# Performance work log

Measured on AMD Instinct MI355X. Metric: run time of the kernel, lower is better.

Reference implementation:

```python
import jax, jax.numpy as jnp
import numpy as np

B, C_IN, H, W = 32, 12, 495, 436
C_HID = 16


def setup_inputs() -> dict:
    key = jax.random.key(0)
    k_x, k1, k2, k3, kb1, kb2, kb3 = jax.random.split(key, 7)
    x = jax.random.uniform(k_x, (B, C_IN, H, W), dtype=jnp.float32) * 255.0
    # Kaiming-uniform-ish init; exact distribution irrelevant for a correctness baseline.
    def u(k, shape, fan_in):
        bound = 1.0 / np.sqrt(fan_in)
        return jax.random.uniform(k, shape, dtype=jnp.float32, minval=-bound, maxval=bound)
    w1 = u(k1, (C_HID, C_IN), C_IN)   # conv1 1x1 kernel [out, in]
    b1 = u(kb1, (C_HID,), C_IN)
    w2 = u(k2, (C_HID, C_HID), C_HID)
    b2 = u(kb2, (C_HID,), C_HID)
    w3 = u(k3, (1, C_HID), C_HID)
    b3 = u(kb3, (1,), C_HID)
    return {"x": x, "w1": w1, "b1": b1, "w2": w2, "b2": b2, "w3": w3, "b3": b3}


def _conv1x1(x, w, b):
    # x: [B, Cin, H, W], w: [Cout, Cin], b: [Cout]
    return jnp.einsum("bchw,oc->bohw", x, w) + b[None, :, None, None]


def reference(x, w1, b1, w2, b2, w3, b3):
    h = x / 255.0 - 0.5
    h = jax.nn.relu(_conv1x1(h, w1, b1))
    h = jax.nn.relu(_conv1x1(h, w2, b2))
    h = jax.nn.sigmoid(_conv1x1(h, w3, b3))
    return 255.0 * h
```

## Files before the change

### kernel.cpp

```cpp
#include <hip/hip_runtime.h>
#include <math.h>

#define B_    32
#define C_IN  12
#define C_HID 16
#define H_    495
#define W_    436
#define HW    (H_ * W_)
#define NPIX  (B_ * HW)
#define NG    (NPIX / 4)

__global__ __launch_bounds__(256) void temporal_mlp_kernel(
    const float* __restrict__ x,
    const float* __restrict__ w1, const float* __restrict__ b1,
    const float* __restrict__ w2, const float* __restrict__ b2,
    const float* __restrict__ w3, const float* __restrict__ b3,
    float* __restrict__ out)
{
    __shared__ __align__(16) float sW1[16][12];
    __shared__ __align__(16) float sB1[16];
    __shared__ __align__(16) float sW2[16][16];
    __shared__ __align__(16) float sB2[16];
    __shared__ __align__(16) float sW3[16];
    __shared__ float sB3;

    const int tid = threadIdx.x;
    if (tid < 192) sW1[tid / 12][tid % 12] = w1[tid] * (1.0f / 255.0f);
    sW2[tid / 16][tid % 16] = w2[tid];
    if (tid < 16) {
        float s = 0.0f;
        #pragma unroll
        for (int c = 0; c < 12; ++c) s += w1[tid * 12 + c];
        sB1[tid] = b1[tid] - 0.5f * s;
        sB2[tid] = b2[tid];
        sW3[tid] = w3[tid];
    }
    if (tid == 0) sB3 = b3[0];
    __syncthreads();

    const int g = blockIdx.x * 256 + tid;
    if (g >= NG) return;

    const int base = g * 4;
    const int b    = base / HW;
    const int p    = base - b * HW;
    const float* xb = x + (size_t)b * (C_IN * HW) + p;

    float xin0[12], xin1[12], xin2[12], xin3[12];
    #pragma unroll
    for (int c = 0; c < 12; ++c) {
        float4 t = *(const float4*)(xb + (size_t)c * HW);
        xin0[c] = t.x; xin1[c] = t.y; xin2[c] = t.z; xin3[c] = t.w;
    }

    float h10[16], h11[16], h12[16], h13[16];
    #pragma unroll
    for (int o = 0; o < 16; ++o) {
        float wr[12];
        ((float4*)wr)[0] = ((const float4*)(&sW1[o][0]))[0];
        ((float4*)wr)[1] = ((const float4*)(&sW1[o][0]))[1];
        ((float4*)wr)[2] = ((const float4*)(&sW1[o][0]))[2];
        const float bb = sB1[o];
        float a0 = bb, a1 = bb, a2 = bb, a3 = bb;
        #pragma unroll
        for (int c = 0; c < 12; ++c) {
            a0 = fmaf(xin0[c], wr[c], a0);
            a1 = fmaf(xin1[c], wr[c], a1);
            a2 = fmaf(xin2[c], wr[c], a2);
            a3 = fmaf(xin3[c], wr[c], a3);
        }
        h10[o] = fmaxf(a0, 0.0f); h11[o] = fmaxf(a1, 0.0f);
        h12[o] = fmaxf(a2, 0.0f); h13[o] = fmaxf(a3, 0.0f);
    }

    float h20[16], h21[16], h22[16], h23[16];
    #pragma unroll
    for (int o = 0; o < 16; ++o) {
        float wr[16];
        ((float4*)wr)[0] = ((const float4*)(&sW2[o][0]))[0];
        ((float4*)wr)[1] = ((const float4*)(&sW2[o][0]))[1];
        ((float4*)wr)[2] = ((const float4*)(&sW2[o][0]))[2];
        ((float4*)wr)[3] = ((const float4*)(&sW2[o][0]))[3];
        const float bb = sB2[o];
        float a0 = bb, a1 = bb, a2 = bb, a3 = bb;
        #pragma unroll
        for (int c = 0; c < 16; ++c) {
            a0 = fmaf(h10[c], wr[c], a0);
            a1 = fmaf(h11[c], wr[c], a1);
            a2 = fmaf(h12[c], wr[c], a2);
            a3 = fmaf(h13[c], wr[c], a3);
        }
        h20[o] = fmaxf(a0, 0.0f); h21[o] = fmaxf(a1, 0.0f);
        h22[o] = fmaxf(a2, 0.0f); h23[o] = fmaxf(a3, 0.0f);
    }

    float wr[16];
    ((float4*)wr)[0] = ((const float4*)(&sW3[0]))[0];
    ((float4*)wr)[1] = ((const float4*)(&sW3[0]))[1];
    ((float4*)wr)[2] = ((const float4*)(&sW3[0]))[2];
    ((float4*)wr)[3] = ((const float4*)(&sW3[0]))[3];
    const float b3v = sB3;
    float t0 = b3v, t1 = b3v, t2 = b3v, t3 = b3v;
    #pragma unroll
    for (int c = 0; c < 16; ++c) {
        t0 = fmaf(h20[c], wr[c], t0);
        t1 = fmaf(h21[c], wr[c], t1);
        t2 = fmaf(h22[c], wr[c], t2);
        t3 = fmaf(h23[c], wr[c], t3);
    }
    float4 r;
    r.x = 255.0f / (1.0f + __expf(-t0));
    r.y = 255.0f / (1.0f + __expf(-t1));
    r.z = 255.0f / (1.0f + __expf(-t2));
    r.w = 255.0f / (1.0f + __expf(-t3));
    *(float4*)(out + base) = r;
}

extern "C" void kernel_launch(void* const* d_in, const int* in_sizes, int n_in,
                              void* d_out, int out_size, void* d_ws, size_t ws_size,
                              hipStream_t stream) {
    const float* x  = (const float*)d_in[0];
    const float* w1 = (const float*)d_in[1];
    const float* b1 = (const float*)d_in[2];
    const float* w2 = (const float*)d_in[3];
    const float* b2 = (const float*)d_in[4];
    const float* w3 = (const float*)d_in[5];
    const float* b3 = (const float*)d_in[6];
    float* out = (float*)d_out;

    const int grid = (NG + 255) / 256;
    temporal_mlp_kernel<<<grid, 256, 0, stream>>>(x, w1, b1, w2, b2, w3, b3, out);
}
```

Measured before the change: 451.9 us.

## Process two pixels per thread and read weights directly from global memory

```diff
diff --git a/kernel.cpp b/kernel.cpp
--- a/kernel.cpp
+++ b/kernel.cpp
@@ -8,7 +8,7 @@
 #define W_    436
 #define HW    (H_ * W_)
 #define NPIX  (B_ * HW)
-#define NG    (NPIX / 4)
+#define NG2   (NPIX / 2)
 
 __global__ __launch_bounds__(256) void temporal_mlp_kernel(
     const float* __restrict__ x,
@@ -17,103 +17,64 @@
     const float* __restrict__ w3, const float* __restrict__ b3,
     float* __restrict__ out)
 {
-    __shared__ __align__(16) float sW1[16][12];
-    __shared__ __align__(16) float sB1[16];
-    __shared__ __align__(16) float sW2[16][16];
-    __shared__ __align__(16) float sB2[16];
-    __shared__ __align__(16) float sW3[16];
-    __shared__ float sB3;
+    const int g = blockIdx.x * 256 + threadIdx.x;
+    if (g >= NG2) return;
 
-    const int tid = threadIdx.x;
-    if (tid < 192) sW1[tid / 12][tid % 12] = w1[tid] * (1.0f / 255.0f);
-    sW2[tid / 16][tid % 16] = w2[tid];
-    if (tid < 16) {
-        float s = 0.0f;
-        #pragma unroll
-        for (int c = 0; c < 12; ++c) s += w1[tid * 12 + c];
-        sB1[tid] = b1[tid] - 0.5f * s;
-        sB2[tid] = b2[tid];
-        sW3[tid] = w3[tid];
-    }
-    if (tid == 0) sB3 = b3[0];
-    __syncthreads();
-
-    const int g = blockIdx.x * 256 + tid;
-    if (g >= NG) return;
-
-    const int base = g * 4;
+    const int base = g * 2;
     const int b    = base / HW;
     const int p    = base - b * HW;
     const float* xb = x + (size_t)b * (C_IN * HW) + p;
 
-    float xin0[12], xin1[12], xin2[12], xin3[12];
+    float xn0[12], xn1[12];
     #pragma unroll
     for (int c = 0; c < 12; ++c) {
-        float4 t = *(const float4*)(xb + (size_t)c * HW);
-        xin0[c] = t.x; xin1[c] = t.y; xin2[c] = t.z; xin3[c] = t.w;
+        float2 t = *(const float2*)(xb + (size_t)c * HW);
+        xn0[c] = fmaf(t.x, 1.0f / 255.0f, -0.5f);
+        xn1[c] = fmaf(t.y, 1.0f / 255.0f, -0.5f);
     }
 
-    float h10[16], h11[16], h12[16], h13[16];
+    float h10[16], h11[16];
     #pragma unroll
     for (int o = 0; o < 16; ++o) {
-        float wr[12];
-        ((float4*)wr)[0] = ((const float4*)(&sW1[o][0]))[0];
-        ((float4*)wr)[1] = ((const float4*)(&sW1[o][0]))[1];
-        ((float4*)wr)[2] = ((const float4*)(&sW1[o][0]))[2];
-        const float bb = sB1[o];
-        float a0 = bb, a1 = bb, a2 = bb, a3 = bb;
+        const float bb = b1[o];
+        float a0 = bb, a1 = bb;
         #pragma unroll
         for (int c = 0; c < 12; ++c) {
-            a0 = fmaf(xin0[c], wr[c], a0);
-            a1 = fmaf(xin1[c], wr[c], a1);
-            a2 = fmaf(xin2[c], wr[c], a2);
-            a3 = fmaf(xin3[c], wr[c], a3);
+            const float w = w1[o * 12 + c];
+            a0 = fmaf(xn0[c], w, a0);
+            a1 = fmaf(xn1[c], w, a1);
         }
-        h10[o] = fmaxf(a0, 0.0f); h11[o] = fmaxf(a1, 0.0f);
-        h12[o] = fmaxf(a2, 0.0f); h13[o] = fmaxf(a3, 0.0f);
+        h10[o] = fmaxf(a0, 0.0f);
+        h11[o] = fmaxf(a1, 0.0f);
     }
 
-    float h20[16], h21[16], h22[16], h23[16];
+    float h20[16], h21[16];
     #pragma unroll
     for (int o = 0; o < 16; ++o) {
-        float wr[16];
-        ((float4*)wr)[0] = ((const float4*)(&sW2[o][0]))[0];
-        ((float4*)wr)[1] = ((const float4*)(&sW2[o][0]))[1];
-        ((float4*)wr)[2] = ((const float4*)(&sW2[o][0]))[2];
-        ((float4*)wr)[3] = ((const float4*)(&sW2[o][0]))[3];
-        const float bb = sB2[o];
-        float a0 = bb, a1 = bb, a2 = bb, a3 = bb;
+        const float bb = b2[o];
+        float a0 = bb, a1 = bb;
         #pragma unroll
         for (int c = 0; c < 16; ++c) {
-            a0 = fmaf(h10[c], wr[c], a0);
-            a1 = fmaf(h11[c], wr[c], a1);
-            a2 = fmaf(h12[c], wr[c], a2);
-            a3 = fmaf(h13[c], wr[c], a3);
+            const float w = w2[o * 16 + c];
+            a0 = fmaf(h10[c], w, a0);
+            a1 = fmaf(h11[c], w, a1);
         }
-        h20[o] = fmaxf(a0, 0.0f); h21[o] = fmaxf(a1, 0.0f);
-        h22[o] = fmaxf(a2, 0.0f); h23[o] = fmaxf(a3, 0.0f);
+        h20[o] = fmaxf(a0, 0.0f);
+        h21[o] = fmaxf(a1, 0.0f);
     }
 
-    float wr[16];
-    ((float4*)wr)[0] = ((const float4*)(&sW3[0]))[0];
-    ((float4*)wr)[1] = ((const float4*)(&sW3[0]))[1];
-    ((float4*)wr)[2] = ((const float4*)(&sW3[0]))[2];
-    ((float4*)wr)[3] = ((const float4*)(&sW3[0]))[3];
-    const float b3v = sB3;
-    float t0 = b3v, t1 = b3v, t2 = b3v, t3 = b3v;
+    float t0 = b3[0], t1 = b3[0];
     #pragma unroll
     for (int c = 0; c < 16; ++c) {
-        t0 = fmaf(h20[c], wr[c], t0);
-        t1 = fmaf(h21[c], wr[c], t1);
-        t2 = fmaf(h22[c], wr[c], t2);
-        t3 = fmaf(h23[c], wr[c], t3);
+        const float w = w3[c];
+        t0 = fmaf(h20[c], w, t0);
+        t1 = fmaf(h21[c], w, t1);
     }
-    float4 r;
-    r.x = 255.0f / (1.0f + __expf(-t0));
-    r.y = 255.0f / (1.0f + __expf(-t1));
-    r.z = 255.0f / (1.0f + __expf(-t2));
-    r.w = 255.0f / (1.0f + __expf(-t3));
-    *(float4*)(out + base) = r;
+
+    float2 r;
+    r.x = 255.0f / (1.0f + expf(-t0));
+    r.y = 255.0f / (1.0f + expf(-t1));
+    *(float2*)(out + base) = r;
 }
 
 extern "C" void kernel_launch(void* const* d_in, const int* in_sizes, int n_in,
@@ -128,6 +89,6 @@
     const float* b3 = (const float*)d_in[6];
     float* out = (float*)d_out;
 
-    const int grid = (NG + 255) / 256;
+    const int grid = (NG2 + 255) / 256;
     temporal_mlp_kernel<<<grid, 256, 0, stream>>>(x, w1, b1, w2, b2, w3, b3, out);
 }
```

After: 466.8 us. +3.3%, slower.
